# Optimization experiments

Hardware: AMD Instinct MI355X
Metric: run time of the kernel (lower is better)

The kernel has to match this reference:

```python
import jax, jax.numpy as jnp
import numpy as np

DIM = 1024
N_HEADS = 16
HEAD_DIM = DIM // N_HEADS
WINDOW = 64


def setup_inputs() -> dict:
    key = jax.random.key(0)
    k1, k2, k3 = jax.random.split(key, 3)
    B, N = 4, 8192
    x = jax.random.normal(k1, (B, N, DIM), dtype=jnp.float32)
    w_qkv = jax.random.normal(k2, (3 * DIM, DIM), dtype=jnp.float32) * (1.0 / np.sqrt(DIM))
    b_qkv = jnp.zeros((3 * DIM,), dtype=jnp.float32)
    w_proj = jax.random.normal(k3, (DIM, DIM), dtype=jnp.float32) * (1.0 / np.sqrt(DIM))
    b_proj = jnp.zeros((DIM,), dtype=jnp.float32)
    return {"x": x, "w_qkv": w_qkv, "b_qkv": b_qkv, "w_proj": w_proj, "b_proj": b_proj}


def reference(x, w_qkv, b_qkv, w_proj, b_proj):
    B, N, C = x.shape
    H, D, W = N_HEADS, HEAD_DIM, WINDOW
    # qkv projection: torch Linear => x @ W.T + b
    qkv = x @ w_qkv.T + b_qkv                      # [B, N, 3C]
    qkv = qkv.reshape(B, N, 3, H, D).transpose(2, 0, 3, 1, 4)  # [3, B, H, N, D]
    q, k, v = qkv[0], qkv[1], qkv[2]               # each [B, H, N, D]
    n_w = N // W                                    # N chosen divisible by window
    # split sequence into non-overlapping windows (block-diagonal attention)
    qw = q.reshape(B, H, n_w, W, D)
    kw = k.reshape(B, H, n_w, W, D)
    vw = v.reshape(B, H, n_w, W, D)
    scale = 1.0 / np.sqrt(D)
    attn = jnp.einsum('bhnqd,bhnkd->bhnqk', qw, kw) * scale  # [B,H,n_w,W,W]
    attn = jax.nn.softmax(attn, axis=-1)
    out = jnp.einsum('bhnqk,bhnkd->bhnqd', attn, vw)          # [B,H,n_w,W,D]
    out = out.reshape(B, H, N, D).transpose(0, 2, 1, 3).reshape(B, N, C)
    return out @ w_proj.T + b_proj
```

## Files before the change

### kernel.cpp

```cpp
#include <hip/hip_runtime.h>
#include <hip/hip_bf16.h>
#include <cstdint>
#include <cstddef>


typedef __attribute__((ext_vector_type(8))) short short8;
typedef __attribute__((ext_vector_type(4))) float float4v;

static __device__ __forceinline__ void async16(void* lds, const void* g) {
  __builtin_amdgcn_global_load_lds((const __attribute__((address_space(1))) void*)g,
                                   (__attribute__((address_space(3))) void*)lds,
                                   16, 0, 0);
}

static __device__ __forceinline__ unsigned short f2bf_bits(float x) {
  unsigned int u = __float_as_uint(x);
  unsigned int r = (u + 0x7fffu + ((u >> 16) & 1u)) >> 16;
  return (unsigned short)r;
}

__global__ __launch_bounds__(256) void cast_f32_to_bf16(
    const float* __restrict__ in, unsigned short* __restrict__ out, int n4) {
  int i = blockIdx.x * 256 + threadIdx.x;
  if (i >= n4) return;
  float4 v = ((const float4*)in)[i];
  ushort4 o;
  o.x = f2bf_bits(v.x); o.y = f2bf_bits(v.y);
  o.z = f2bf_bits(v.z); o.w = f2bf_bits(v.w);
  ((ushort4*)out)[i] = o;
}

template<bool OUT_BF16>
__global__ __launch_bounds__(256) void gemm_bt(
    const unsigned short* __restrict__ A,
    const unsigned short* __restrict__ B,
    const float* __restrict__ bias,
    void* __restrict__ Cout,
    int M, int N, int K, int ntiles)
{
  __shared__ unsigned short As[128 * 32];
  __shared__ unsigned short Bs[128 * 32];

  const int t    = threadIdx.x;
  const int wave = t >> 6;
  const int lane = t & 63;

  const int GM    = 8;
  const int group = blockIdx.x / (GM * ntiles);
  const int inG   = blockIdx.x % (GM * ntiles);
  const int bm    = group * GM + (inG % GM);
  const int bn    = inG / GM;

  const int wm   = (wave >> 1) * 64;
  const int wn   = (wave & 1) * 64;
  const int lr   = lane & 15;
  const int lk   = (lane >> 4) * 8;

  const int srow = t >> 2;
  const int scol = (t & 3) << 3;
  const unsigned short* Ag = A + (size_t)(bm * 128 + srow) * K + scol;
  const unsigned short* Bg = B + (size_t)(bn * 128 + srow) * K + scol;
  unsigned short* Asw = As + wave * 512;
  unsigned short* Bsw = Bs + wave * 512;

  float4v acc[4][4];
  #pragma unroll
  for (int i = 0; i < 4; ++i)
    #pragma unroll
    for (int j = 0; j < 4; ++j) acc[i][j] = (float4v){0.f, 0.f, 0.f, 0.f};

  for (int k0 = 0; k0 < K; k0 += 32) {
    async16(Asw,        Ag + k0);
    async16(Asw + 2048, Ag + (size_t)64 * K + k0);
    async16(Bsw,        Bg + k0);
    async16(Bsw + 2048, Bg + (size_t)64 * K + k0);
    __syncthreads();

    short8 af[4], bfr[4];
    #pragma unroll
    for (int i = 0; i < 4; ++i)
      af[i] = *(const short8*)(As + (wm + i * 16 + lr) * 32 + lk);
    #pragma unroll
    for (int j = 0; j < 4; ++j)
      bfr[j] = *(const short8*)(Bs + (wn + j * 16 + lr) * 32 + lk);
    #pragma unroll
    for (int i = 0; i < 4; ++i)
      #pragma unroll
      for (int j = 0; j < 4; ++j)
        acc[i][j] = __builtin_amdgcn_mfma_f32_16x16x32_bf16(af[i], bfr[j], acc[i][j], 0, 0, 0);
    __syncthreads();
  }

  const int rbase = bm * 128 + wm + (lane >> 4) * 4;
  const int cbase = bn * 128 + wn + lr;
  #pragma unroll
  for (int j = 0; j < 4; ++j) {
    const int col = cbase + j * 16;
    const float bv = bias[col];
    #pragma unroll
    for (int i = 0; i < 4; ++i) {
      const int row = rbase + i * 16;
      #pragma unroll
      for (int r = 0; r < 4; ++r) {
        float v = acc[i][j][r] + bv;
        if (OUT_BF16)
          ((unsigned short*)Cout)[(size_t)(row + r) * N + col] = f2bf_bits(v);
        else
          ((float*)Cout)[(size_t)(row + r) * N + col] = v;
      }
    }
  }
}

__global__ __launch_bounds__(256) void win_attn(
    const unsigned short* __restrict__ qkv,
    unsigned short* __restrict__ out)
{
  __shared__ unsigned short Qs[64 * 64];
  __shared__ unsigned short Ks[64 * 64];
  __shared__ unsigned short Vt[64 * 64];
  __shared__ unsigned short Ps[64 * 64];

  const int t    = threadIdx.x;
  const int wave = t >> 6;
  const int lane = t & 63;
  const int wid  = blockIdx.x;
  const int h    = (wid >> 7) & 15;
  const int b    = wid >> 11;
  const int wi   = wid & 127;
  const int tok0 = b * 8192 + wi * 64;

  const unsigned short* qb = qkv + (size_t)tok0 * 3072 + h * 64;
  const unsigned short* kb = qb + 1024;
  const unsigned short* vb = qb + 2048;

  {
    const int row = t >> 3;
    const int col = (t & 7) << 3;
    unsigned short* Qw = Qs + wave * 512;
    unsigned short* Kw = Ks + wave * 512;
    #pragma unroll
    for (int o = 0; o < 2; ++o) {
      async16(Qw + o * 2048, qb + (size_t)(o * 32 + row) * 3072 + col);
      async16(Kw + o * 2048, kb + (size_t)(o * 32 + row) * 3072 + col);
    }
    const int key = lane;
    const int d0  = wave * 8;
    #pragma unroll
    for (int o = 0; o < 2; ++o) {
      const int d = d0 + o * 32;
      ushort4 r0 = *(const ushort4*)(vb + (size_t)key * 3072 + d);
      ushort4 r1 = *(const ushort4*)(vb + (size_t)key * 3072 + d + 4);
      Vt[(d + 0) * 64 + key] = r0.x; Vt[(d + 1) * 64 + key] = r0.y;
      Vt[(d + 2) * 64 + key] = r0.z; Vt[(d + 3) * 64 + key] = r0.w;
      Vt[(d + 4) * 64 + key] = r1.x; Vt[(d + 5) * 64 + key] = r1.y;
      Vt[(d + 6) * 64 + key] = r1.z; Vt[(d + 7) * 64 + key] = r1.w;
    }
  }
  __syncthreads();

  const int lr = lane & 15;
  const int lq = lane >> 4;

  short8 qa[2];
  #pragma unroll
  for (int k2 = 0; k2 < 2; ++k2)
    qa[k2] = *(const short8*)(Qs + (wave * 16 + lr) * 64 + k2 * 32 + lq * 8);

  float4v s[4];
  #pragma unroll
  for (int jt = 0; jt < 4; ++jt) {
    float4v a = (float4v){0.f, 0.f, 0.f, 0.f};
    #pragma unroll
    for (int k2 = 0; k2 < 2; ++k2) {
      short8 kf = *(const short8*)(Ks + (jt * 16 + lr) * 64 + k2 * 32 + lq * 8);
      a = __builtin_amdgcn_mfma_f32_16x16x32_bf16(qa[k2], kf, a, 0, 0, 0);
    }
    s[jt] = a;
  }

  const float scale = 0.125f;
  float pr[4][4];
  #pragma unroll
  for (int r = 0; r < 4; ++r) {
    float m = s[0][r];
    #pragma unroll
    for (int jt = 1; jt < 4; ++jt) m = fmaxf(m, s[jt][r]);
    #pragma unroll
    for (int off = 1; off < 16; off <<= 1) m = fmaxf(m, __shfl_xor(m, off));
    float sum = 0.f;
    #pragma unroll
    for (int jt = 0; jt < 4; ++jt) {
      float e = __expf((s[jt][r] - m) * scale);
      pr[jt][r] = e; sum += e;
    }
    #pragma unroll
    for (int off = 1; off < 16; off <<= 1) sum += __shfl_xor(sum, off);
    float inv = 1.0f / sum;
    #pragma unroll
    for (int jt = 0; jt < 4; ++jt) pr[jt][r] *= inv;
  }

  #pragma unroll
  for (int jt = 0; jt < 4; ++jt)
    #pragma unroll
    for (int r = 0; r < 4; ++r)
      Ps[(wave * 16 + lq * 4 + r) * 64 + jt * 16 + lr] = f2bf_bits(pr[jt][r]);
  __syncthreads();

  short8 pa[2];
  #pragma unroll
  for (int k2 = 0; k2 < 2; ++k2)
    pa[k2] = *(const short8*)(Ps + (wave * 16 + lr) * 64 + k2 * 32 + lq * 8);

  unsigned short* ob = out + h * 64;
  #pragma unroll
  for (int jd = 0; jd < 4; ++jd) {
    float4v a = (float4v){0.f, 0.f, 0.f, 0.f};
    #pragma unroll
    for (int k2 = 0; k2 < 2; ++k2) {
      short8 vf = *(const short8*)(Vt + (jd * 16 + lr) * 64 + k2 * 32 + lq * 8);
      a = __builtin_amdgcn_mfma_f32_16x16x32_bf16(pa[k2], vf, a, 0, 0, 0);
    }
    #pragma unroll
    for (int r = 0; r < 4; ++r) {
      const int row = wave * 16 + lq * 4 + r;
      ob[(size_t)(tok0 + row) * 1024 + jd * 16 + lr] = f2bf_bits(a[r]);
    }
  }
}

extern "C" void kernel_launch(void* const* d_in, const int* in_sizes, int n_in,
                              void* d_out, int out_size, void* d_ws, size_t ws_size,
                              hipStream_t stream) {
  const float* x      = (const float*)d_in[0];
  const float* w_qkv  = (const float*)d_in[1];
  const float* b_qkv  = (const float*)d_in[2];
  const float* w_proj = (const float*)d_in[3];
  const float* b_proj = (const float*)d_in[4];
  float* outp = (float*)d_out;

  char* ws = (char*)d_ws;
  unsigned short* xb     = (unsigned short*)(ws);
  unsigned short* wqkvb  = (unsigned short*)(ws + 67108864);
  unsigned short* wprojb = (unsigned short*)(ws + 73400320);
  unsigned short* qkvb   = (unsigned short*)(ws + 75497472);
  unsigned short* attnb  = (unsigned short*)(ws + 276824064);

  cast_f32_to_bf16<<<32768, 256, 0, stream>>>(x,      xb,     33554432 / 4);
  cast_f32_to_bf16<<<3072,  256, 0, stream>>>(w_qkv,  wqkvb,  3145728 / 4);
  cast_f32_to_bf16<<<1024,  256, 0, stream>>>(w_proj, wprojb, 1048576 / 4);

  gemm_bt<true><<<256 * 24, 256, 0, stream>>>(xb, wqkvb, b_qkv, qkvb,
                                              32768, 3072, 1024, 24);
  win_attn<<<8192, 256, 0, stream>>>(qkvb, attnb);
  gemm_bt<false><<<256 * 8, 256, 0, stream>>>(attnb, wprojb, b_proj, outp,
                                              32768, 1024, 1024, 8);
}
```

Baseline: 655.9 us.

## Replace GEMM with 256x256-tile, double-buffered, swizzled 8-wave pipelined kernel

Replaces the 128x128, single-buffered GEMM with a 256x256-tile kernel that uses 8 waves, 128 KiB of dynamic LDS double-buffered across K steps, an XOR-swizzled LDS layout, and explicit vmcnt waits with raw barriers. Loads for the next K tiles are interleaved with four MFMA phases, with wave priority raised during the math. Block ordering is remapped across 8 groups (likely per XCD) to improve cache locality. The goal is more reuse per tile and overlap of global loads with MFMA work, at the cost of heavy LDS and register use and a fragile hand-written barrier and wait ordering.

```diff
diff --git a/kernel.cpp b/kernel.cpp
--- a/kernel.cpp
+++ b/kernel.cpp
@@ -7,9 +7,9 @@
 typedef __attribute__((ext_vector_type(8))) short short8;
 typedef __attribute__((ext_vector_type(4))) float float4v;
 
-static __device__ __forceinline__ void async16(void* lds, const void* g) {
+static __device__ __forceinline__ void async16(void* lds_p, const void* g) {
   __builtin_amdgcn_global_load_lds((const __attribute__((address_space(1))) void*)g,
-                                   (__attribute__((address_space(3))) void*)lds,
+                                   (__attribute__((address_space(3))) void*)lds_p,
                                    16, 0, 0);
 }
 
@@ -18,6 +18,9 @@
   unsigned int r = (u + 0x7fffu + ((u >> 16) & 1u)) >> 16;
   return (unsigned short)r;
 }
+
+#define S_BARRIER() asm volatile("s_barrier" ::: "memory")
+#define WAIT_VM(n)  asm volatile("s_waitcnt vmcnt(" #n ")" ::: "memory")
 
 __global__ __launch_bounds__(256) void cast_f32_to_bf16(
     const float* __restrict__ in, unsigned short* __restrict__ out, int n4) {
@@ -31,78 +34,164 @@
 }
 
 template<bool OUT_BF16>
-__global__ __launch_bounds__(256) void gemm_bt(
+__global__ __launch_bounds__(512, 2) void gemm256(
     const unsigned short* __restrict__ A,
     const unsigned short* __restrict__ B,
     const float* __restrict__ bias,
     void* __restrict__ Cout,
     int M, int N, int K, int ntiles)
 {
-  __shared__ unsigned short As[128 * 32];
-  __shared__ unsigned short Bs[128 * 32];
+  extern __shared__ unsigned short lds[];
 
   const int t    = threadIdx.x;
   const int wave = t >> 6;
   const int lane = t & 63;
-
-  const int GM    = 8;
-  const int group = blockIdx.x / (GM * ntiles);
-  const int inG   = blockIdx.x % (GM * ntiles);
+  const int lr   = lane & 15;
+  const int lq   = lane >> 4;
+  const int wm   = wave >> 2;
+  const int wn   = wave & 3;
+
+  const int nwg  = gridDim.x;
+  const int q8   = nwg >> 3;
+  const int wg   = ((int)blockIdx.x & 7) * q8 + ((int)blockIdx.x >> 3);
+  const int GM   = 8;
+  const int group = wg / (GM * ntiles);
+  const int inG   = wg % (GM * ntiles);
   const int bm    = group * GM + (inG % GM);
   const int bn    = inG / GM;
 
-  const int wm   = (wave >> 1) * 64;
-  const int wn   = (wave & 1) * 64;
-  const int lr   = lane & 15;
-  const int lk   = (lane >> 4) * 8;
-
-  const int srow = t >> 2;
-  const int scol = (t & 3) << 3;
-  const unsigned short* Ag = A + (size_t)(bm * 128 + srow) * K + scol;
-  const unsigned short* Bg = B + (size_t)(bn * 128 + srow) * K + scol;
-  unsigned short* Asw = As + wave * 512;
-  unsigned short* Bsw = Bs + wave * 512;
-
-  float4v acc[4][4];
-  #pragma unroll
-  for (int i = 0; i < 4; ++i)
+  const int srow = t >> 3;
+  const int sswz = ((t & 7) ^ (srow & 7)) << 3;
+  const unsigned short* Abase = A + (size_t)(bm * 256 + srow) * K + sswz;
+  const unsigned short* Bbase = B + (size_t)(bn * 256 + srow) * K + sswz;
+  const int ldsw = wave * 512;
+
+  auto stageA = [&](int kt, int c) {
+    async16(lds + (kt & 1) * 16384 + c * 4096 + ldsw,
+            Abase + (size_t)(c * 64) * K + kt * 64);
+  };
+  auto stageB = [&](int kt, int c) {
+    async16(lds + 32768 + (kt & 1) * 16384 + c * 4096 + ldsw,
+            Bbase + (size_t)(c * 64) * K + kt * 64);
+  };
+
+  const int g0 = ((0 + lq) ^ (lr & 7)) << 3;
+  const int g1 = ((4 + lq) ^ (lr & 7)) << 3;
+  const int arow0 = (wm * 128 + lr) * 64;
+  const int brow0 = (wn * 64 + lr) * 64;
+
+  float4v acc[8][4];
+  #pragma unroll
+  for (int i = 0; i < 8; ++i)
     #pragma unroll
     for (int j = 0; j < 4; ++j) acc[i][j] = (float4v){0.f, 0.f, 0.f, 0.f};
 
-  for (int k0 = 0; k0 < K; k0 += 32) {
-    async16(Asw,        Ag + k0);
-    async16(Asw + 2048, Ag + (size_t)64 * K + k0);
-    async16(Bsw,        Bg + k0);
-    async16(Bsw + 2048, Bg + (size_t)64 * K + k0);
-    __syncthreads();
-
-    short8 af[4], bfr[4];
-    #pragma unroll
-    for (int i = 0; i < 4; ++i)
-      af[i] = *(const short8*)(As + (wm + i * 16 + lr) * 32 + lk);
-    #pragma unroll
-    for (int j = 0; j < 4; ++j)
-      bfr[j] = *(const short8*)(Bs + (wn + j * 16 + lr) * 32 + lk);
-    #pragma unroll
-    for (int i = 0; i < 4; ++i)
-      #pragma unroll
-      for (int j = 0; j < 4; ++j)
-        acc[i][j] = __builtin_amdgcn_mfma_f32_16x16x32_bf16(af[i], bfr[j], acc[i][j], 0, 0, 0);
-    __syncthreads();
-  }
-
-  const int rbase = bm * 128 + wm + (lane >> 4) * 4;
-  const int cbase = bn * 128 + wn + lr;
-  #pragma unroll
-  for (int j = 0; j < 4; ++j) {
-    const int col = cbase + j * 16;
+  const int NT = K >> 6;
+
+  #pragma unroll
+  for (int c = 0; c < 4; ++c) stageB(0, c);
+  #pragma unroll
+  for (int c = 0; c < 4; ++c) stageA(0, c);
+  #pragma unroll
+  for (int c = 0; c < 4; ++c) stageB(1, c);
+  WAIT_VM(4);
+  S_BARRIER();
+
+  short8 af[4][2], bf[2][2], bf2[2][2];
+
+  for (int kt = 0; kt < NT; ++kt) {
+    const int bc = kt & 1;
+    int kt1 = kt + 1; if (kt1 == NT) kt1 = 0;
+    int kt2 = kt + 2; if (kt2 >= NT) kt2 -= NT;
+    const unsigned short* Al = lds + bc * 16384;
+    const unsigned short* Bl = lds + 32768 + bc * 16384;
+
+    #pragma unroll
+    for (int mf = 0; mf < 4; ++mf) {
+      af[mf][0] = *(const short8*)(Al + arow0 + mf * 1024 + g0);
+      af[mf][1] = *(const short8*)(Al + arow0 + mf * 1024 + g1);
+    }
+    #pragma unroll
+    for (int nf = 0; nf < 2; ++nf) {
+      bf[nf][0] = *(const short8*)(Bl + brow0 + nf * 1024 + g0);
+      bf[nf][1] = *(const short8*)(Bl + brow0 + nf * 1024 + g1);
+    }
+    stageA(kt1, 0); stageA(kt1, 2);
+    S_BARRIER();
+    __builtin_amdgcn_s_setprio(1);
+    #pragma unroll
+    for (int mf = 0; mf < 4; ++mf)
+      #pragma unroll
+      for (int nf = 0; nf < 2; ++nf) {
+        acc[mf][nf] = __builtin_amdgcn_mfma_f32_16x16x32_bf16(af[mf][0], bf[nf][0], acc[mf][nf], 0, 0, 0);
+        acc[mf][nf] = __builtin_amdgcn_mfma_f32_16x16x32_bf16(af[mf][1], bf[nf][1], acc[mf][nf], 0, 0, 0);
+      }
+    __builtin_amdgcn_s_setprio(0);
+    S_BARRIER();
+
+    #pragma unroll
+    for (int nf = 0; nf < 2; ++nf) {
+      bf2[nf][0] = *(const short8*)(Bl + brow0 + (2 + nf) * 1024 + g0);
+      bf2[nf][1] = *(const short8*)(Bl + brow0 + (2 + nf) * 1024 + g1);
+    }
+    stageA(kt1, 1); stageA(kt1, 3);
+    S_BARRIER();
+    __builtin_amdgcn_s_setprio(1);
+    #pragma unroll
+    for (int mf = 0; mf < 4; ++mf)
+      #pragma unroll
+      for (int nf = 0; nf < 2; ++nf) {
+        acc[mf][2 + nf] = __builtin_amdgcn_mfma_f32_16x16x32_bf16(af[mf][0], bf2[nf][0], acc[mf][2 + nf], 0, 0, 0);
+        acc[mf][2 + nf] = __builtin_amdgcn_mfma_f32_16x16x32_bf16(af[mf][1], bf2[nf][1], acc[mf][2 + nf], 0, 0, 0);
+      }
+    __builtin_amdgcn_s_setprio(0);
+    S_BARRIER();
+
+    #pragma unroll
+    for (int mf = 0; mf < 4; ++mf) {
+      af[mf][0] = *(const short8*)(Al + arow0 + (4 + mf) * 1024 + g0);
+      af[mf][1] = *(const short8*)(Al + arow0 + (4 + mf) * 1024 + g1);
+    }
+    stageB(kt2, 0); stageB(kt2, 1);
+    S_BARRIER();
+    __builtin_amdgcn_s_setprio(1);
+    #pragma unroll
+    for (int mf = 0; mf < 4; ++mf)
+      #pragma unroll
+      for (int nf = 0; nf < 2; ++nf) {
+        acc[4 + mf][nf] = __builtin_amdgcn_mfma_f32_16x16x32_bf16(af[mf][0], bf[nf][0], acc[4 + mf][nf], 0, 0, 0);
+        acc[4 + mf][nf] = __builtin_amdgcn_mfma_f32_16x16x32_bf16(af[mf][1], bf[nf][1], acc[4 + mf][nf], 0, 0, 0);
+      }
+    __builtin_amdgcn_s_setprio(0);
+    S_BARRIER();
+
+    stageB(kt2, 2); stageB(kt2, 3);
+    WAIT_VM(4);
+    S_BARRIER();
+    __builtin_amdgcn_s_setprio(1);
+    #pragma unroll
+    for (int mf = 0; mf < 4; ++mf)
+      #pragma unroll
+      for (int nf = 0; nf < 2; ++nf) {
+        acc[4 + mf][2 + nf] = __builtin_amdgcn_mfma_f32_16x16x32_bf16(af[mf][0], bf2[nf][0], acc[4 + mf][2 + nf], 0, 0, 0);
+        acc[4 + mf][2 + nf] = __builtin_amdgcn_mfma_f32_16x16x32_bf16(af[mf][1], bf2[nf][1], acc[4 + mf][2 + nf], 0, 0, 0);
+      }
+    __builtin_amdgcn_s_setprio(0);
+    S_BARRIER();
+  }
+
+  const int rbase = bm * 256 + wm * 128 + lq * 4;
+  const int cbase = bn * 256 + wn * 64 + lr;
+  #pragma unroll
+  for (int nf = 0; nf < 4; ++nf) {
+    const int col = cbase + nf * 16;
     const float bv = bias[col];
     #pragma unroll
-    for (int i = 0; i < 4; ++i) {
-      const int row = rbase + i * 16;
+    for (int mf = 0; mf < 8; ++mf) {
+      const int row = rbase + mf * 16;
       #pragma unroll
       for (int r = 0; r < 4; ++r) {
-        float v = acc[i][j][r] + bv;
+        float v = acc[mf][nf][r] + bv;
         if (OUT_BF16)
           ((unsigned short*)Cout)[(size_t)(row + r) * N + col] = f2bf_bits(v);
         else
@@ -247,13 +336,22 @@
   unsigned short* qkvb   = (unsigned short*)(ws + 75497472);
   unsigned short* attnb  = (unsigned short*)(ws + 276824064);
 
+  static int attr_done = 0;
+  if (!attr_done) {
+    hipFuncSetAttribute(reinterpret_cast<const void*>(&gemm256<true>),
+                        hipFuncAttributeMaxDynamicSharedMemorySize, 131072);
+    hipFuncSetAttribute(reinterpret_cast<const void*>(&gemm256<false>),
+                        hipFuncAttributeMaxDynamicSharedMemorySize, 131072);
+    attr_done = 1;
+  }
+
   cast_f32_to_bf16<<<32768, 256, 0, stream>>>(x,      xb,     33554432 / 4);
   cast_f32_to_bf16<<<3072,  256, 0, stream>>>(w_qkv,  wqkvb,  3145728 / 4);
   cast_f32_to_bf16<<<1024,  256, 0, stream>>>(w_proj, wprojb, 1048576 / 4);
 
-  gemm_bt<true><<<256 * 24, 256, 0, stream>>>(xb, wqkvb, b_qkv, qkvb,
-                                              32768, 3072, 1024, 24);
+  gemm256<true><<<128 * 12, 512, 131072, stream>>>(xb, wqkvb, b_qkv, qkvb,
+                                                   32768, 3072, 1024, 12);
   win_attn<<<8192, 256, 0, stream>>>(qkvb, attnb);
-  gemm_bt<false><<<256 * 8, 256, 0, stream>>>(attnb, wprojb, b_proj, outp,
-                                              32768, 1024, 1024, 8);
-}
+  gemm256<false><<<128 * 4, 512, 131072, stream>>>(attnb, wprojb, b_proj, outp,
+                                                   32768, 1024, 1024, 4);
+}
```

After: 602.0 us. 8.2% less time.
